# Kernel optimization log

Hardware: AMD Instinct MI355X
Metric: run time of the kernel (lower is better)

The kernel has to match this reference:

```python
import jax, jax.numpy as jnp
import numpy as np

T, B, L, CTX, H = 512, 512, 16, 64, 128
STATE_DIM, SHOT, PID, DATA = 32, 12, 35, 23


def setup_inputs() -> dict:
    key = jax.random.key(0)
    ks = jax.random.split(key, 64)
    k = iter(ks)
    def rn(shape, s=0.1):
        return (jax.random.normal(next(k), shape) * s).astype(jnp.float32)
    xs = jax.random.normal(next(k), (T, B, DATA), jnp.float32)
    xs = xs.at[:, :, 12].set(jax.random.randint(next(k), (T, B), 0, SHOT).astype(jnp.float32))
    xs = xs.at[:, :, 17].set(jax.random.randint(next(k), (T, B), 0, PID).astype(jnp.float32))
    xs = xs.at[:, :, 20].set(jax.random.randint(next(k), (T, B), 0, SHOT).astype(jnp.float32))
    return dict(
        total_xs=jnp.zeros((1,), jnp.float32),
        xs=xs,
        ts=jnp.linspace(0.0, 2.0, T).astype(jnp.float32),
        noise_std=jnp.asarray(0.1, jnp.float32),
        z0_noise=jax.random.normal(next(k), (B, L), jnp.float32),
        bm_noise=jax.random.normal(next(k), (T - 1, B, L), jnp.float32),
        shot_emb=rn((SHOT, 8)), player_emb=rn((PID, 8)),
        gru_wih=rn((3 * H, STATE_DIM)), gru_whh=rn((3 * H, H)),
        gru_bih=rn((3 * H,)), gru_bhh=rn((3 * H,)),
        enc_w=rn((CTX, H)), enc_b=rn((CTX,)),
        qz0_w=rn((2 * L, CTX)), qz0_b=rn((2 * L,)),
        f_w1=rn((H, L + CTX)), f_b1=rn((H,)), f_w2=rn((H, H)), f_b2=rn((H,)),
        f_w3=rn((L, H)), f_b3=rn((L,)),
        h_w1=rn((H, L)), h_b1=rn((H,)), h_w2=rn((H, H)), h_b2=rn((H,)),
        h_w3=rn((L, H)), h_b3=rn((L,)),
        g_w1=rn((L, H)), g_b1=rn((L, H)), g_w2=rn((L, H)), g_b2=rn((L,)),
        proj_w=rn((STATE_DIM, L)), proj_b=rn((STATE_DIM,)),
        pz0_mean=jnp.zeros((1, L), jnp.float32), pz0_logstd=jnp.zeros((1, L), jnp.float32),
        act_w=rn((128, L)), act_b=rn((128,)),
        act_land_w=rn((2, 128)), act_shot_w=rn((SHOT, 128)), act_move_w=rn((2, 128)),
    )


def _forward(xs, noise_std, shot_emb, player_emb, gru_wih, gru_whh, gru_bih, gru_bhh,
             enc_w, enc_b, qz0_w, qz0_b,
             f_w1, f_b1, f_w2, f_b2, f_w3, f_b3,
             h_w1, h_b1, h_w2, h_b2, h_w3, h_b3,
             g_w1, g_b1, g_w2, g_b2,
             proj_w, proj_b, pz0_mean, pz0_logstd,
             act_w, act_b, act_land_w, act_shot_w, act_move_w,
             ts, z0_noise, bm_noise):
    # --- SDE_embed_and_transform: replace shot/player id cols with embeddings ---
    state = xs[:, :, :18]
    shot_ids = state[:, :, 12].astype(jnp.int32)
    pid_ids = state[:, :, 17].astype(jnp.int32)
    state_t = jnp.concatenate([state[:, :, :12], shot_emb[shot_ids],
                               state[:, :, 13:17], player_emb[pid_ids]], axis=-1)  # (T,B,32)
    xs_t = jnp.concatenate([state_t, xs[:, :, 18:]], axis=-1)  # (T,B,37)
    # --- Encoder: GRU over time-reversed states, linear head, flip back ---
    def gru_step(h, xt):
        gi = xt @ gru_wih.T + gru_bih
        gh = h @ gru_whh.T + gru_bhh
        ir, iz, inn = jnp.split(gi, 3, axis=-1)
        hr, hz, hn = jnp.split(gh, 3, axis=-1)
        r = jax.nn.sigmoid(ir + hr)
        zg = jax.nn.sigmoid(iz + hz)
        n = jnp.tanh(inn + r * hn)
        hnew = (1.0 - zg) * n + zg * h
        return hnew, hnew
    h0 = jnp.zeros((xs.shape[1], gru_whh.shape[1]), xs.dtype)
    _, hs = jax.lax.scan(gru_step, h0, state_t[::-1])
    ctx = (hs @ enc_w.T + enc_b)[::-1]  # (T,B,CTX)
    # --- posterior z0 ---
    qm, qls = jnp.split(ctx[0] @ qz0_w.T + qz0_b, 2, axis=1)
    z0 = qm + jnp.exp(qls) * z0_noise
    # --- Euler-Maruyama with logqp; searchsorted(right) -> ctx[min(i+1,T-1)] = ctx[i+1] ---
    dts = ts[1:] - ts[:-1]  # (T-1,)
    dW = jnp.sqrt(dts)[:, None, None] * bm_noise
    ctx_steps = ctx[1:]
    def mlp3(x, w1, b1, w2, b2, w3, b3):
        h1 = jax.nn.softplus(x @ w1.T + b1)
        h2 = jax.nn.softplus(h1 @ w2.T + b2)
        return h2 @ w3.T + b3
    def g_diag(y):  # (B,L): per-latent-dim scalar nets, batched over L
        hg = jax.nn.softplus(y[:, :, None] * g_w1[None] + g_b1[None])  # (B,L,H)
        return jax.nn.sigmoid(jnp.einsum('blh,lh->bl', hg, g_w2) + g_b2)
    def sde_step(z, inp):
        c, dw, dt = inp
        f_val = mlp3(jnp.concatenate([z, c], axis=1), f_w1, f_b1, f_w2, f_b2, f_w3, f_b3)
        h_val = mlp3(z, h_w1, h_b1, h_w2, h_b2, h_w3, h_b3)
        g_val = g_diag(z)
        u = (f_val - h_val) / g_val
        logr = 0.5 * jnp.sum(u * u, axis=1) * dt
        z_new = z + f_val * dt + g_val * dw
        return z_new, (z_new, logr)
    _, (z_tail, log_ratio) = jax.lax.scan(sde_step, z0, (ctx_steps, dW, dts))
    zs = jnp.concatenate([z0[None], z_tail], axis=0)  # (T,B,L)
    _xs = zs @ proj_w.T + proj_b  # (T,B,32)
    # --- action model losses ---
    a = jax.nn.relu(zs @ act_w.T + act_b)
    land = (a @ act_land_w.T).reshape(-1, 2)
    shot_logits = (a @ act_shot_w.T).reshape(-1, act_shot_w.shape[0])
    move = (a @ act_move_w.T).reshape(-1, 2)
    true_actions = xs_t[:, :, -5:]
    true_land = true_actions[:, :, :2].reshape(-1, 2)
    true_move = true_actions[:, :, 3:].reshape(-1, 2)
    true_shot = true_actions[:, :, 2].astype(jnp.int32).reshape(-1)
    land_loss = jnp.mean((land - true_land) ** 2)
    move_loss = jnp.mean((move - true_move) ** 2)
    logp = jax.nn.log_softmax(shot_logits, axis=-1)
    picked = jnp.take_along_axis(logp, true_shot[:, None], axis=1)[:, 0]
    mask = (true_shot != 0).astype(logp.dtype)  # CrossEntropy ignore_index=0
    shot_loss = -jnp.sum(picked * mask) / jnp.maximum(jnp.sum(mask), 1.0)
    # --- reconstruction log-likelihood ---
    xs_state = xs_t[:, :, :STATE_DIM]
    LOG2PI = 1.8378770664093453
    log_pxs = jnp.mean(jnp.sum(
        -0.5 * ((xs_state - _xs) / noise_std) ** 2 - jnp.log(noise_std) - 0.5 * LOG2PI,
        axis=(0, 2)))
    # --- KL(q(z0) || p(z0)) ---
    var_q = jnp.exp(2.0 * qls)
    var_p = jnp.exp(2.0 * pz0_logstd)
    kl = pz0_logstd - qls + (var_q + (qm - pz0_mean) ** 2) / (2.0 * var_p) - 0.5
    logqp0 = jnp.mean(jnp.sum(kl, axis=1))
    logqp_path = jnp.mean(jnp.sum(log_ratio, axis=0))
    return log_pxs, logqp0 + logqp_path + land_loss + shot_loss + move_loss


def reference(total_xs, xs, ts, noise_std, z0_noise, bm_noise, shot_emb, player_emb,
              gru_wih, gru_whh, gru_bih, gru_bhh, enc_w, enc_b, qz0_w, qz0_b,
              f_w1, f_b1, f_w2, f_b2, f_w3, f_b3, h_w1, h_b1, h_w2, h_b2, h_w3, h_b3,
              g_w1, g_b1, g_w2, g_b2, proj_w, proj_b, pz0_mean, pz0_logstd,
              act_w, act_b, act_land_w, act_shot_w, act_move_w):
    return _forward(xs, noise_std, shot_emb, player_emb, gru_wih, gru_whh, gru_bih, gru_bhh,
                    enc_w, enc_b, qz0_w, qz0_b,
                    f_w1, f_b1, f_w2, f_b2, f_w3, f_b3,
                    h_w1, h_b1, h_w2, h_b2, h_w3, h_b3,
                    g_w1, g_b1, g_w2, g_b2,
                    proj_w, proj_b, pz0_mean, pz0_logstd,
                    act_w, act_b, act_land_w, act_shot_w, act_move_w,
                    ts, z0_noise, bm_noise)
```

## Files before the change

kernel.cpp:

```cpp
#include <hip/hip_runtime.h>
#include <cstdint>

typedef _Float16 f16;
typedef _Float16 f16x2 __attribute__((ext_vector_type(2)));

#define T_STEPS 512
#define B_SZ 512
#define LOG2PI 1.8378770664093453f

__device__ __forceinline__ void barrier_lds() {
  asm volatile("s_waitcnt lgkmcnt(0)" ::: "memory");
  __builtin_amdgcn_s_barrier();
  asm volatile("" ::: "memory");
}

__device__ __forceinline__ uint32_t packh2(float a, float b) {
  f16x2 v; v[0] = (f16)a; v[1] = (f16)b;
  return __builtin_bit_cast(uint32_t, v);
}

__device__ __forceinline__ float fdot2(uint32_t a, uint32_t b, float c) {
#if defined(__AMDGCN__) && __has_builtin(__builtin_amdgcn_fdot2)
  return __builtin_amdgcn_fdot2(__builtin_bit_cast(f16x2, a),
                                __builtin_bit_cast(f16x2, b), c, false);
#else
  f16x2 x = __builtin_bit_cast(f16x2, a), y = __builtin_bit_cast(f16x2, b);
  return c + (float)x[0] * (float)y[0] + (float)x[1] * (float)y[1];
#endif
}

#define DOT4(acc, w0, w1, w2, w3, v)                                     \
  do {                                                                   \
    acc = fdot2((w0), (v).x, acc); acc = fdot2((w1), (v).y, acc);        \
    acc = fdot2((w2), (v).z, acc); acc = fdot2((w3), (v).w, acc);        \
  } while (0)

__device__ __forceinline__ float sigmoidf_(float x) {
  return 1.0f / (1.0f + __expf(-x));
}
__device__ __forceinline__ float tanhf_(float x) {
  float ax = fabsf(x);
  float t = __expf(-2.0f * ax);
  float r = (1.0f - t) / (1.0f + t);
  return copysignf(r, x);
}
__device__ __forceinline__ float softplusf_(float x) {
  return fmaxf(x, 0.0f) + __logf(1.0f + __expf(-fabsf(x)));
}

__global__ __launch_bounds__(256) void k_embed(
    const float* __restrict__ xs, const float* __restrict__ shot_emb,
    const float* __restrict__ player_emb, f16* __restrict__ state_t,
    float* __restrict__ accums) {
  if (blockIdx.x == 0 && threadIdx.x < 16) accums[threadIdx.x] = 0.0f;
  size_t idx = (size_t)blockIdx.x * 256 + threadIdx.x;
  const float* xp = xs + idx * 23;
  f16* op = state_t + idx * 32;
  int sid = (int)xp[12];
  int pid = (int)xp[17];
#pragma unroll
  for (int i = 0; i < 12; ++i) op[i] = (f16)xp[i];
  const float* se = shot_emb + sid * 8;
#pragma unroll
  for (int i = 0; i < 8; ++i) op[12 + i] = (f16)se[i];
#pragma unroll
  for (int i = 0; i < 4; ++i) op[20 + i] = (f16)xp[13 + i];
  const float* pe = player_emb + pid * 8;
#pragma unroll
  for (int i = 0; i < 8; ++i) op[24 + i] = (f16)pe[i];
}

__global__ __launch_bounds__(512) void k_gru(
    const f16* __restrict__ state_t, const float* __restrict__ wih,
    const float* __restrict__ whh, const float* __restrict__ bih,
    const float* __restrict__ bhh, const float* __restrict__ enc_w,
    const float* __restrict__ enc_b, const float* __restrict__ qz0_w,
    const float* __restrict__ qz0_b, const float* __restrict__ z0_noise,
    const float* __restrict__ pz0_mean, const float* __restrict__ pz0_logstd,
    f16* __restrict__ ctx, float* __restrict__ z0_out,
    float* __restrict__ accums) {
  __shared__ uint32_t s_x[2][16];
  __shared__ uint32_t s_h[2][64];
  __shared__ float s_gates[2 * 128 * 4];
  __shared__ float s_encp[2 * 64 * 2];
  __shared__ float s_ctx0[2][64];
  __shared__ float s_q[2][32];

  const int tid = threadIdx.x;
  const int bbase = blockIdx.x * 2;
  const uint32_t* stu = (const uint32_t*)state_t;

  uint32_t wA[64];
  uint32_t wB[16];
  float bias0 = 0.f, bias1 = 0.f, encbr = 0.f;

  if (tid < 256) {
    int g = tid >> 7, du = tid & 127;
    const float* whr = whh + (size_t)(g * 128 + du) * 128;
#pragma unroll
    for (int i = 0; i < 64; ++i) wA[i] = packh2(whr[2 * i], whr[2 * i + 1]);
    const float* wxr = wih + (size_t)(g * 128 + du) * 32;
#pragma unroll
    for (int i = 0; i < 16; ++i) wB[i] = packh2(wxr[2 * i], wxr[2 * i + 1]);
    bias0 = bih[g * 128 + du] + bhh[g * 128 + du];
  } else if (tid < 384) {
    int du = tid - 256;
    const float* whr = whh + (size_t)(256 + du) * 128;
#pragma unroll
    for (int i = 0; i < 64; ++i) wA[i] = packh2(whr[2 * i], whr[2 * i + 1]);
    const float* wxr = wih + (size_t)(256 + du) * 32;
#pragma unroll
    for (int i = 0; i < 16; ++i) wB[i] = packh2(wxr[2 * i], wxr[2 * i + 1]);
    bias0 = bih[256 + du];
    bias1 = bhh[256 + du];
  } else {
    int e = tid - 384, c = e & 63, ks = e >> 6;
    const float* wer = enc_w + (size_t)c * 128 + ks * 64;
#pragma unroll
    for (int i = 0; i < 32; ++i) wA[i] = packh2(wer[2 * i], wer[2 * i + 1]);
    encbr = enc_b[c];
  }

  if (tid < 128) s_h[tid >> 6][tid & 63] = 0u;
  if (tid < 32) {
    int b = tid >> 4, i = tid & 15;
    s_x[b][i] = stu[((size_t)(T_STEPS - 1) * B_SZ + bbase + b) * 16 + i];
  }
  float h_old = 0.0f;
  __syncthreads();

  for (int t = T_STEPS - 1; t >= 0; --t) {
    uint4 xpref = make_uint4(0, 0, 0, 0);
    if (tid < 256) {
      int g = tid >> 7, du = tid & 127;
#pragma unroll
      for (int b = 0; b < 2; ++b) {
        float a = bias0;
        const uint4* xq = (const uint4*)&s_x[b][0];
#pragma unroll
        for (int j = 0; j < 4; ++j) {
          uint4 v = xq[j];
          DOT4(a, wB[4 * j], wB[4 * j + 1], wB[4 * j + 2], wB[4 * j + 3], v);
        }
        const uint4* hq = (const uint4*)&s_h[b][0];
#pragma unroll
        for (int j = 0; j < 16; ++j) {
          uint4 v = hq[j];
          DOT4(a, wA[4 * j], wA[4 * j + 1], wA[4 * j + 2], wA[4 * j + 3], v);
        }
        s_gates[(b * 128 + du) * 4 + g] = a;
      }
    } else if (tid < 384) {
      int du = tid - 256;
#pragma unroll
      for (int b = 0; b < 2; ++b) {
        float aI = bias0, aH = bias1;
        const uint4* xq = (const uint4*)&s_x[b][0];
#pragma unroll
        for (int j = 0; j < 4; ++j) {
          uint4 v = xq[j];
          DOT4(aI, wB[4 * j], wB[4 * j + 1], wB[4 * j + 2], wB[4 * j + 3], v);
        }
        const uint4* hq = (const uint4*)&s_h[b][0];
#pragma unroll
        for (int j = 0; j < 16; ++j) {
          uint4 v = hq[j];
          DOT4(aH, wA[4 * j], wA[4 * j + 1], wA[4 * j + 2], wA[4 * j + 3], v);
        }
        s_gates[(b * 128 + du) * 4 + 2] = aI;
        s_gates[(b * 128 + du) * 4 + 3] = aH;
      }
    } else {
      int e = tid - 384, ks = e >> 6, cc = e & 63;
      (void)cc;
      if (t < T_STEPS - 1) {
#pragma unroll
        for (int b = 0; b < 2; ++b) {
          float a = 0.f;
          const uint4* hq = (const uint4*)&s_h[b][ks * 32];
#pragma unroll
          for (int j = 0; j < 8; ++j) {
            uint4 v = hq[j];
            DOT4(a, wA[4 * j], wA[4 * j + 1], wA[4 * j + 2], wA[4 * j + 3], v);
          }
          s_encp[(b * 64 + cc) * 2 + ks] = a;
        }
      }
      if (e < 8 && t > 0) {
        int b = e & 1, q = e >> 1;
        xpref = *(const uint4*)(stu +
                                ((size_t)(t - 1) * B_SZ + bbase + b) * 16 + q * 4);
      }
    }
    barrier_lds();
    if (tid < 256) {
      int b = tid >> 7, du = tid & 127;
      const float4 gt = *(const float4*)&s_gates[(b * 128 + du) * 4];
      float r = sigmoidf_(gt.x), zg = sigmoidf_(gt.y);
      float n = tanhf_(gt.z + r * gt.w);
      float hnew = (1.0f - zg) * n + zg * h_old;
      h_old = hnew;
      ((f16*)&s_h[b][0])[du] = (f16)hnew;
    } else if (tid >= 384) {
      int e = tid - 384, cc = e & 63, b = e >> 6;
      if (t < T_STEPS - 1) {
        float2 p = *(const float2*)&s_encp[(b * 64 + cc) * 2];
        ctx[((size_t)(t + 1) * B_SZ + bbase + b) * 64 + cc] =
            (f16)(p.x + p.y + encbr);
      }
      if (e < 8 && t > 0) {
        int b2 = e & 1, q = e >> 1;
        *(uint4*)&s_x[b2][q * 4] = xpref;
      }
    }
    barrier_lds();
  }

  if (tid >= 384) {
    int e = tid - 384, ks = e >> 6, cc = e & 63;
#pragma unroll
    for (int b = 0; b < 2; ++b) {
      float a = 0.f;
      const uint4* hq = (const uint4*)&s_h[b][ks * 32];
#pragma unroll
      for (int j = 0; j < 8; ++j) {
        uint4 v = hq[j];
        DOT4(a, wA[4 * j], wA[4 * j + 1], wA[4 * j + 2], wA[4 * j + 3], v);
      }
      s_encp[(b * 64 + cc) * 2 + ks] = a;
    }
  }
  __syncthreads();
  if (tid >= 384) {
    int e = tid - 384, cc = e & 63, b = e >> 6;
    float2 p = *(const float2*)&s_encp[(b * 64 + cc) * 2];
    float val = p.x + p.y + encbr;
    ctx[((size_t)bbase + b) * 64 + cc] = (f16)val;
    s_ctx0[b][cc] = val;
  }
  __syncthreads();
  if (tid < 64) {
    int b = tid >> 5, o = tid & 31;
    float acc = qz0_b[o];
#pragma unroll 8
    for (int k = 0; k < 64; ++k) acc += qz0_w[o * 64 + k] * s_ctx0[b][k];
    s_q[b][o] = acc;
  }
  __syncthreads();
  if (tid < 32) {
    int b = tid >> 4, l = tid & 15;
    int bg = bbase + b;
    float qm = s_q[b][l], qls = s_q[b][16 + l];
    float z0v = qm + __expf(qls) * z0_noise[bg * 16 + l];
    z0_out[bg * 16 + l] = z0v;
    float pm = pz0_mean[l], pls = pz0_logstd[l];
    float var_q = __expf(2.0f * qls);
    float var_p = __expf(2.0f * pls);
    float dm = qm - pm;
    float kl = pls - qls + (var_q + dm * dm) / (2.0f * var_p) - 0.5f;
    atomicAdd(&accums[5], kl);
  }
}

__global__ __launch_bounds__(256, 2) void k_sde(
    const f16* __restrict__ ctx, const float* __restrict__ z0_in,
    const float* __restrict__ ts, const float* __restrict__ bm_noise,
    const float* __restrict__ fw1, const float* __restrict__ fb1,
    const float* __restrict__ fw2, const float* __restrict__ fb2,
    const float* __restrict__ fw3, const float* __restrict__ fb3,
    const float* __restrict__ hw1, const float* __restrict__ hb1,
    const float* __restrict__ hw2, const float* __restrict__ hb2,
    const float* __restrict__ hw3, const float* __restrict__ hb3,
    const float* __restrict__ gw1, const float* __restrict__ gb1,
    const float* __restrict__ gw2, const float* __restrict__ gb2,
    f16* __restrict__ zs, float* __restrict__ accums) {
  __shared__ uint32_t s_x2[40];
  __shared__ float s_zf[16];
  __shared__ uint32_t s_h1[2][64];
  __shared__ uint32_t s_h2[2][64];
  __shared__ float s_gp[256];
  __shared__ float s_dts[T_STEPS];

  const int tid = threadIdx.x;
  const int bg = blockIdx.x;
  const uint32_t* cu = (const uint32_t*)ctx;

  uint32_t gw1r[8], gb1r[8], gw2r[8];
  uint32_t uw1[40];
  uint32_t wP2[64];
  uint32_t wP3[32];
  float bias1r = 0.f, bias2r = 0.f, gb2r = 0.f, fb3r = 0.f, hb3r = 0.f;

  {
    int l = tid & 15, kc = tid >> 4;
#pragma unroll
    for (int i = 0; i < 8; ++i) {
      int h = kc * 8 + i;
      gw1r[i] = __builtin_bit_cast(uint32_t, gw1[l * 128 + h]);
      gb1r[i] = __builtin_bit_cast(uint32_t, gb1[l * 128 + h]);
      gw2r[i] = __builtin_bit_cast(uint32_t, gw2[l * 128 + h]);
    }
  }
  if (tid < 128) {
    const float* w = fw1 + (size_t)tid * 80;
#pragma unroll
    for (int i = 0; i < 40; ++i) uw1[i] = packh2(w[2 * i], w[2 * i + 1]);
    bias1r = fb1[tid];
  } else {
    int u = tid - 128;
    const float* w = hw1 + (size_t)u * 16;
#pragma unroll
    for (int i = 0; i < 8; ++i) uw1[i] = packh2(w[2 * i], w[2 * i + 1]);
    bias1r = hb1[u];
  }
  {
    int mlp = tid >> 7, u = tid & 127;
    const float* w = (mlp ? hw2 : fw2) + (size_t)u * 128;
#pragma unroll
    for (int i = 0; i < 64; ++i) wP2[i] = packh2(w[2 * i], w[2 * i + 1]);
    bias2r = (mlp ? hb2 : fb2)[u];
  }
  if (tid < 64) {
    int l = tid >> 2, mlp = (tid >> 1) & 1, kh = tid & 1;
    const float* w = (mlp ? hw3 : fw3) + (size_t)l * 128 + kh * 64;
#pragma unroll
    for (int i = 0; i < 32; ++i) wP3[i] = packh2(w[2 * i], w[2 * i + 1]);
    if ((tid & 3) == 0) {
      gb2r = gb2[l];
      fb3r = fb3[l];
      hb3r = hb3[l];
    }
  }

  for (int i = tid; i < T_STEPS - 1; i += 256) s_dts[i] = ts[i + 1] - ts[i];
  float bmc = 0.f;
  float path_acc = 0.0f;
  uint4 cpref = make_uint4(0, 0, 0, 0);
  if (tid < 64 && (tid & 3) == 0) {
    int l = tid >> 2;
    float z = z0_in[bg * 16 + l];
    s_zf[l] = z;
    ((f16*)&s_x2[0])[l] = (f16)z;
    zs[(size_t)bg * 16 + l] = (f16)z;
    bmc = bm_noise[(size_t)bg * 16 + l];
  }
  if (tid >= 128 && tid < 136) {
    int q = tid - 128;
    uint4 v = *(const uint4*)(cu + ((size_t)1 * B_SZ + bg) * 32 + q * 4);
    *(uint4*)&s_x2[8 + q * 4] = v;
  }
  __syncthreads();

  for (int t = 0; t < T_STEPS - 1; ++t) {
    float bmn = 0.f;
    if (tid < 64 && (tid & 3) == 0 && t < T_STEPS - 2)
      bmn = bm_noise[((size_t)(t + 1) * B_SZ + bg) * 16 + (tid >> 2)];
    if (tid >= 128 && tid < 136 && t <= T_STEPS - 3) {
      int q = tid - 128;
      cpref = *(const uint4*)(cu + ((size_t)(t + 2) * B_SZ + bg) * 32 + q * 4);
    }
    {
      int l = tid & 15;
      float y = s_zf[l];
      float acc = 0.f;
#pragma unroll
      for (int i = 0; i < 8; ++i) {
        float pre = fmaf(y, __builtin_bit_cast(float, gw1r[i]),
                         __builtin_bit_cast(float, gb1r[i]));
        acc = fmaf(softplusf_(pre), __builtin_bit_cast(float, gw2r[i]), acc);
      }
      s_gp[l * 16 + (tid >> 4)] = acc;
    }
    if (tid < 128) {
      float a0 = bias1r, a1 = 0.f;
      const uint4* xq = (const uint4*)&s_x2[0];
#pragma unroll
      for (int j = 0; j < 10; j += 2) {
        uint4 v0 = xq[j], v1 = xq[j + 1];
        DOT4(a0, uw1[4 * j], uw1[4 * j + 1], uw1[4 * j + 2], uw1[4 * j + 3], v0);
        DOT4(a1, uw1[4 * j + 4], uw1[4 * j + 5], uw1[4 * j + 6], uw1[4 * j + 7], v1);
      }
      ((f16*)&s_h1[0][0])[tid] = (f16)softplusf_(a0 + a1);
    } else {
      float a = bias1r;
      const uint4* xq = (const uint4*)&s_x2[0];
#pragma unroll
      for (int j = 0; j < 2; ++j) {
        uint4 v = xq[j];
        DOT4(a, uw1[4 * j], uw1[4 * j + 1], uw1[4 * j + 2], uw1[4 * j + 3], v);
      }
      ((f16*)&s_h1[1][0])[tid - 128] = (f16)softplusf_(a);
    }
    barrier_lds();
    {
      int mlp = tid >> 7, u = tid & 127;
      float a0 = 0.f, a1 = 0.f;
      const uint4* hq = (const uint4*)&s_h1[mlp][0];
#pragma unroll
      for (int j = 0; j < 16; j += 2) {
        uint4 v0 = hq[j], v1 = hq[j + 1];
        DOT4(a0, wP2[4 * j], wP2[4 * j + 1], wP2[4 * j + 2], wP2[4 * j + 3], v0);
        DOT4(a1, wP2[4 * j + 4], wP2[4 * j + 5], wP2[4 * j + 6], wP2[4 * j + 7], v1);
      }
      ((f16*)&s_h2[mlp][0])[u] = (f16)softplusf_(a0 + a1 + bias2r);
    }
    barrier_lds();
    if (tid < 64) {
      int l = tid >> 2, kh = tid & 1;
      int mlp = (tid >> 1) & 1;
      const uint4* hq = (const uint4*)&s_h2[mlp][kh * 32];
      float a0 = 0.f, a1 = 0.f;
#pragma unroll
      for (int j = 0; j < 8; j += 2) {
        uint4 v0 = hq[j], v1 = hq[j + 1];
        DOT4(a0, wP3[4 * j], wP3[4 * j + 1], wP3[4 * j + 2], wP3[4 * j + 3], v0);
        DOT4(a1, wP3[4 * j + 4], wP3[4 * j + 5], wP3[4 * j + 6], wP3[4 * j + 7], v1);
      }
      float a = a0 + a1;
      float full = a + __shfl_xor(a, 1);
      float other = __shfl_xor(full, 2);
      if ((tid & 3) == 0) {
        float fv = full + fb3r;
        float hv = other + hb3r;
        const float4* gp = (const float4*)&s_gp[l * 16];
        float4 g0 = gp[0], g1 = gp[1], g2 = gp[2], g3 = gp[3];
        float gs = g0.x + g0.y + g0.z + g0.w + g1.x + g1.y + g1.z + g1.w +
                   g2.x + g2.y + g2.z + g2.w + g3.x + g3.y + g3.z + g3.w + gb2r;
        float gv = sigmoidf_(gs);
        float dt = s_dts[t];
        float u_ = (fv - hv) / gv;
        float lsum = u_ * u_;
        lsum += __shfl_xor(lsum, 4);
        lsum += __shfl_xor(lsum, 8);
        lsum += __shfl_xor(lsum, 16);
        lsum += __shfl_xor(lsum, 32);
        if (tid == 0) path_acc += 0.5f * lsum * dt;
        float dw = sqrtf(dt) * bmc;
        float zn = s_zf[l] + fv * dt + gv * dw;
        s_zf[l] = zn;
        ((f16*)&s_x2[0])[l] = (f16)zn;
        zs[((size_t)(t + 1) * B_SZ + bg) * 16 + l] = (f16)zn;
        bmc = bmn;
      }
    } else if (tid >= 128 && tid < 136 && t <= T_STEPS - 3) {
      int q = tid - 128;
      *(uint4*)&s_x2[8 + q * 4] = cpref;
    }
    barrier_lds();
  }
  if (tid == 0) atomicAdd(&accums[6], path_acc);
}

__global__ __launch_bounds__(256) void k_dec(
    const f16* __restrict__ zs, const f16* __restrict__ state_t,
    const float* __restrict__ xs, const float* __restrict__ proj_w,
    const float* __restrict__ proj_b, const float* __restrict__ act_w,
    const float* __restrict__ act_b, const float* __restrict__ land_w,
    const float* __restrict__ shot_w, const float* __restrict__ move_w,
    float* __restrict__ accums) {
  __shared__ uint32_t s_proj[8 * 32];
  __shared__ uint32_t s_act[8 * 128];
  __shared__ uint32_t s_head[128 * 8];
  __shared__ float s_pb[32], s_ab[128];
  __shared__ float s_red[4 * 5];

  const int tid = threadIdx.x;
  for (int id = tid; id < 8 * 32; id += 256) {
    int kp = id & 7, n = id >> 3;
    s_proj[kp * 32 + n] = packh2(proj_w[n * 16 + 2 * kp], proj_w[n * 16 + 2 * kp + 1]);
  }
  for (int id = tid; id < 8 * 128; id += 256) {
    int kp = id & 7, n = id >> 3;
    s_act[kp * 128 + n] = packh2(act_w[n * 16 + 2 * kp], act_w[n * 16 + 2 * kp + 1]);
  }
  for (int id = tid; id < 128 * 8; id += 256) {
    int j = id >> 3, p = id & 7;
    int h0 = 2 * p, h1 = 2 * p + 1;
    float w0 = (h0 < 2) ? land_w[h0 * 128 + j]
                        : (h0 < 14 ? shot_w[(h0 - 2) * 128 + j]
                                   : move_w[(h0 - 14) * 128 + j]);
    float w1 = (h1 < 2) ? land_w[h1 * 128 + j]
                        : (h1 < 14 ? shot_w[(h1 - 2) * 128 + j]
                                   : move_w[(h1 - 14) * 128 + j]);
    s_head[j * 8 + p] = packh2(w0, w1);
  }
  if (tid < 32) s_pb[tid] = proj_b[tid];
  if (tid < 128) s_ab[tid] = act_b[tid];
  __syncthreads();

  size_t idx = (size_t)blockIdx.x * 256 + tid;
  uint32_t z2[8];
  const uint32_t* zp = (const uint32_t*)(zs + idx * 16);
#pragma unroll
  for (int i = 0; i < 8; ++i) z2[i] = zp[i];
  uint32_t stv[16];
  const uint32_t* stp = (const uint32_t*)(state_t + idx * 32);
#pragma unroll
  for (int i = 0; i < 16; ++i) stv[i] = stp[i];

  float sqsum = 0.0f;
#pragma unroll 4
  for (int i = 0; i < 32; ++i) {
    float acc = s_pb[i];
#pragma unroll
    for (int kp = 0; kp < 8; ++kp) acc = fdot2(s_proj[kp * 32 + i], z2[kp], acc);
    f16x2 sv = __builtin_bit_cast(f16x2, stv[i >> 1]);
    float d = (float)sv[i & 1] - acc;
    sqsum += d * d;
  }

  float hd[16];
#pragma unroll
  for (int i = 0; i < 16; ++i) hd[i] = 0.0f;
#pragma unroll 2
  for (int j = 0; j < 128; ++j) {
    float a = s_ab[j];
#pragma unroll
    for (int kp = 0; kp < 8; ++kp) a = fdot2(s_act[kp * 128 + j], z2[kp], a);
    a = fmaxf(a, 0.0f);
#pragma unroll
    for (int p = 0; p < 8; ++p) {
      f16x2 w = __builtin_bit_cast(f16x2, s_head[j * 8 + p]);
      hd[2 * p] += (float)w[0] * a;
      hd[2 * p + 1] += (float)w[1] * a;
    }
  }
  const float* xp = xs + idx * 23;
  float dl0 = hd[0] - xp[18], dl1 = hd[1] - xp[19];
  float land = dl0 * dl0 + dl1 * dl1;
  float dm0 = hd[14] - xp[21], dm1 = hd[15] - xp[22];
  float move = dm0 * dm0 + dm1 * dm1;
  int sid = (int)xp[20];
  float m = hd[2];
#pragma unroll
  for (int s = 1; s < 12; ++s) m = fmaxf(m, hd[2 + s]);
  float sume = 0.0f;
#pragma unroll
  for (int s = 0; s < 12; ++s) sume += __expf(hd[2 + s] - m);
  float lse = m + __logf(sume);
  float pl = 0.0f;
#pragma unroll
  for (int s = 0; s < 12; ++s)
    if (s == sid) pl = hd[2 + s];
  float picked = 0.0f, cnt = 0.0f;
  if (sid != 0) {
    picked = pl - lse;
    cnt = 1.0f;
  }
  float vals[5] = {sqsum, land, move, picked, cnt};
#pragma unroll
  for (int v = 0; v < 5; ++v) {
    float x = vals[v];
    for (int off = 1; off < 64; off <<= 1) x += __shfl_xor(x, off);
    vals[v] = x;
  }
  int lane = tid & 63, wv = tid >> 6;
  if (lane == 0) {
#pragma unroll
    for (int v = 0; v < 5; ++v) s_red[wv * 5 + v] = vals[v];
  }
  __syncthreads();
  if (tid == 0) {
#pragma unroll
    for (int v = 0; v < 5; ++v) {
      float s = s_red[v] + s_red[5 + v] + s_red[10 + v] + s_red[15 + v];
      atomicAdd(&accums[v], s);
    }
  }
}

__global__ void k_fin(const float* __restrict__ accums,
                      const float* __restrict__ noise_std,
                      float* __restrict__ out) {
  if (threadIdx.x == 0 && blockIdx.x == 0) {
    float sd = noise_std[0];
    float log_pxs = -0.5f * accums[0] / (sd * sd * (float)B_SZ) -
                    (float)T_STEPS * 32.0f * (logf(sd) + 0.5f * LOG2PI);
    float land = accums[1] / (float)(T_STEPS * B_SZ * 2);
    float move = accums[2] / (float)(T_STEPS * B_SZ * 2);
    float shot = -accums[3] / fmaxf(accums[4], 1.0f);
    float out1 = accums[5] / (float)B_SZ + accums[6] / (float)B_SZ + land + shot + move;
    out[0] = log_pxs;
    out[1] = out1;
  }
}

extern "C" void kernel_launch(void* const* d_in, const int* in_sizes, int n_in,
                              void* d_out, int out_size, void* d_ws,
                              size_t ws_size, hipStream_t stream) {
  const float* xs = (const float*)d_in[1];
  const float* ts = (const float*)d_in[2];
  const float* noise_std = (const float*)d_in[3];
  const float* z0_noise = (const float*)d_in[4];
  const float* bm_noise = (const float*)d_in[5];
  const float* shot_emb = (const float*)d_in[6];
  const float* player_emb = (const float*)d_in[7];
  const float* gru_wih = (const float*)d_in[8];
  const float* gru_whh = (const float*)d_in[9];
  const float* gru_bih = (const float*)d_in[10];
  const float* gru_bhh = (const float*)d_in[11];
  const float* enc_w = (const float*)d_in[12];
  const float* enc_b = (const float*)d_in[13];
  const float* qz0_w = (const float*)d_in[14];
  const float* qz0_b = (const float*)d_in[15];
  const float* f_w1 = (const float*)d_in[16];
  const float* f_b1 = (const float*)d_in[17];
  const float* f_w2 = (const float*)d_in[18];
  const float* f_b2 = (const float*)d_in[19];
  const float* f_w3 = (const float*)d_in[20];
  const float* f_b3 = (const float*)d_in[21];
  const float* h_w1 = (const float*)d_in[22];
  const float* h_b1 = (const float*)d_in[23];
  const float* h_w2 = (const float*)d_in[24];
  const float* h_b2 = (const float*)d_in[25];
  const float* h_w3 = (const float*)d_in[26];
  const float* h_b3 = (const float*)d_in[27];
  const float* g_w1 = (const float*)d_in[28];
  const float* g_b1 = (const float*)d_in[29];
  const float* g_w2 = (const float*)d_in[30];
  const float* g_b2 = (const float*)d_in[31];
  const float* proj_w = (const float*)d_in[32];
  const float* proj_b = (const float*)d_in[33];
  const float* pz0_mean = (const float*)d_in[34];
  const float* pz0_logstd = (const float*)d_in[35];
  const float* act_w = (const float*)d_in[36];
  const float* act_b = (const float*)d_in[37];
  const float* act_land_w = (const float*)d_in[38];
  const float* act_shot_w = (const float*)d_in[39];
  const float* act_move_w = (const float*)d_in[40];

  char* ws = (char*)d_ws;
  float* accums = (float*)ws;
  f16* state_t = (f16*)(ws + 256);
  f16* ctx = (f16*)(ws + 256 + 16777216);
  float* z0b = (float*)(ws + 256 + 16777216 + 33554432);
  f16* zs = (f16*)(ws + 256 + 16777216 + 33554432 + 32768);

  k_embed<<<1024, 256, 0, stream>>>(xs, shot_emb, player_emb, state_t, accums);
  k_gru<<<256, 512, 0, stream>>>(state_t, gru_wih, gru_whh, gru_bih, gru_bhh,
                                 enc_w, enc_b, qz0_w, qz0_b, z0_noise, pz0_mean,
                                 pz0_logstd, ctx, z0b, accums);
  k_sde<<<512, 256, 0, stream>>>(ctx, z0b, ts, bm_noise, f_w1, f_b1, f_w2, f_b2,
                                 f_w3, f_b3, h_w1, h_b1, h_w2, h_b2, h_w3, h_b3,
                                 g_w1, g_b1, g_w2, g_b2, zs, accums);
  k_dec<<<1024, 256, 0, stream>>>(zs, state_t, xs, proj_w, proj_b, act_w, act_b,
                                  act_land_w, act_shot_w, act_move_w, accums);
  k_fin<<<1, 64, 0, stream>>>(accums, noise_std, (float*)d_out);
}
```

Before: 1.934 ms.

## Run SDE solver per batch element in a single wavefront without barriers

Rewrites the SDE integration kernel to use one 64-lane wavefront per batch element instead of 256 threads. Each lane computes two hidden units, so every per-timestep block barrier can be dropped and only compiler memory fences remain. Layer-1, layer-3 and diffusion-net weights move from registers to LDS, while the layer-2 weights (256 packed registers per lane) stay in registers. This removes barrier latency on the serial 511-step critical path, at the cost of more work per lane and high register pressure that could spill.

After: 3.219 ms. 1.66x slower.

```diff
diff --git a/kernel.cpp b/kernel.cpp
--- a/kernel.cpp
+++ b/kernel.cpp
@@ -46,6 +46,9 @@
 }
 __device__ __forceinline__ float softplusf_(float x) {
   return fmaxf(x, 0.0f) + __logf(1.0f + __expf(-fabsf(x)));
+}
+__device__ __forceinline__ float asf_(uint32_t u) {
+  return __builtin_bit_cast(float, u);
 }
 
 __global__ __launch_bounds__(256) void k_embed(
@@ -262,7 +265,7 @@
   }
 }
 
-__global__ __launch_bounds__(256, 2) void k_sde(
+__global__ __launch_bounds__(64, 1) void k_sde(
     const f16* __restrict__ ctx, const float* __restrict__ z0_in,
     const float* __restrict__ ts, const float* __restrict__ bm_noise,
     const float* __restrict__ fw1, const float* __restrict__ fb1,
@@ -274,181 +277,223 @@
     const float* __restrict__ gw1, const float* __restrict__ gb1,
     const float* __restrict__ gw2, const float* __restrict__ gb2,
     f16* __restrict__ zs, float* __restrict__ accums) {
-  __shared__ uint32_t s_x2[40];
+  __shared__ uint4 f1w[64][21];
+  __shared__ uint4 h1w[64][5];
+  __shared__ uint4 f3w[64][5];
+  __shared__ uint4 h3w[64][5];
+  __shared__ uint4 gB[64][25];
+  __shared__ uint4 x2s[10];
+  __shared__ uint4 h1f[16], h1h[16], h2f[16], h2h[16];
   __shared__ float s_zf[16];
-  __shared__ uint32_t s_h1[2][64];
-  __shared__ uint32_t s_h2[2][64];
-  __shared__ float s_gp[256];
   __shared__ float s_dts[T_STEPS];
 
-  const int tid = threadIdx.x;
+  const int ln = threadIdx.x;
   const int bg = blockIdx.x;
-  const uint32_t* cu = (const uint32_t*)ctx;
-
-  uint32_t gw1r[8], gb1r[8], gw2r[8];
-  uint32_t uw1[40];
-  uint32_t wP2[64];
-  uint32_t wP3[32];
-  float bias1r = 0.f, bias2r = 0.f, gb2r = 0.f, fb3r = 0.f, hb3r = 0.f;
+  const int l = ln >> 2, kc = ln & 3;
+  const int r0 = 2 * ln, r1 = 2 * ln + 1;
 
   {
-    int l = tid & 15, kc = tid >> 4;
+    uint32_t* p = (uint32_t*)&f1w[ln][0];
+    const float* wa = fw1 + (size_t)r0 * 80;
+    const float* wb = fw1 + (size_t)r1 * 80;
+#pragma unroll
+    for (int i = 0; i < 40; ++i) {
+      p[i] = packh2(wa[2 * i], wa[2 * i + 1]);
+      p[40 + i] = packh2(wb[2 * i], wb[2 * i + 1]);
+    }
+  }
+  {
+    uint32_t* p = (uint32_t*)&h1w[ln][0];
+    const float* wa = hw1 + (size_t)r0 * 16;
+    const float* wb = hw1 + (size_t)r1 * 16;
 #pragma unroll
     for (int i = 0; i < 8; ++i) {
-      int h = kc * 8 + i;
-      gw1r[i] = __builtin_bit_cast(uint32_t, gw1[l * 128 + h]);
-      gb1r[i] = __builtin_bit_cast(uint32_t, gb1[l * 128 + h]);
-      gw2r[i] = __builtin_bit_cast(uint32_t, gw2[l * 128 + h]);
-    }
-  }
-  if (tid < 128) {
-    const float* w = fw1 + (size_t)tid * 80;
-#pragma unroll
-    for (int i = 0; i < 40; ++i) uw1[i] = packh2(w[2 * i], w[2 * i + 1]);
-    bias1r = fb1[tid];
-  } else {
-    int u = tid - 128;
-    const float* w = hw1 + (size_t)u * 16;
-#pragma unroll
-    for (int i = 0; i < 8; ++i) uw1[i] = packh2(w[2 * i], w[2 * i + 1]);
-    bias1r = hb1[u];
+      p[i] = packh2(wa[2 * i], wa[2 * i + 1]);
+      p[8 + i] = packh2(wb[2 * i], wb[2 * i + 1]);
+    }
   }
   {
-    int mlp = tid >> 7, u = tid & 127;
-    const float* w = (mlp ? hw2 : fw2) + (size_t)u * 128;
-#pragma unroll
-    for (int i = 0; i < 64; ++i) wP2[i] = packh2(w[2 * i], w[2 * i + 1]);
-    bias2r = (mlp ? hb2 : fb2)[u];
-  }
-  if (tid < 64) {
-    int l = tid >> 2, mlp = (tid >> 1) & 1, kh = tid & 1;
-    const float* w = (mlp ? hw3 : fw3) + (size_t)l * 128 + kh * 64;
-#pragma unroll
-    for (int i = 0; i < 32; ++i) wP3[i] = packh2(w[2 * i], w[2 * i + 1]);
-    if ((tid & 3) == 0) {
-      gb2r = gb2[l];
-      fb3r = fb3[l];
-      hb3r = hb3[l];
-    }
-  }
-
-  for (int i = tid; i < T_STEPS - 1; i += 256) s_dts[i] = ts[i + 1] - ts[i];
-  float bmc = 0.f;
-  float path_acc = 0.0f;
+    uint32_t* p = (uint32_t*)&f3w[ln][0];
+    uint32_t* q = (uint32_t*)&h3w[ln][0];
+    const float* wa = fw3 + (size_t)l * 128 + kc * 32;
+    const float* wb = hw3 + (size_t)l * 128 + kc * 32;
+#pragma unroll
+    for (int i = 0; i < 16; ++i) {
+      p[i] = packh2(wa[2 * i], wa[2 * i + 1]);
+      q[i] = packh2(wb[2 * i], wb[2 * i + 1]);
+    }
+  }
+  {
+    float* gp = (float*)&gB[ln][0];
+    const int hb = kc * 32;
+#pragma unroll
+    for (int j = 0; j < 32; ++j) {
+      gp[j] = gw1[l * 128 + hb + j];
+      gp[32 + j] = gb1[l * 128 + hb + j];
+      gp[64 + j] = gw2[l * 128 + hb + j];
+    }
+  }
+  uint4 f2a[16], f2b[16], h2a[16], h2b[16];
+  {
+    const float* wa = fw2 + (size_t)r0 * 128;
+    const float* wb = fw2 + (size_t)r1 * 128;
+    const float* wc = hw2 + (size_t)r0 * 128;
+    const float* wd = hw2 + (size_t)r1 * 128;
+#pragma unroll
+    for (int j = 0; j < 16; ++j) {
+      uint4 u;
+      u.x = packh2(wa[8 * j + 0], wa[8 * j + 1]);
+      u.y = packh2(wa[8 * j + 2], wa[8 * j + 3]);
+      u.z = packh2(wa[8 * j + 4], wa[8 * j + 5]);
+      u.w = packh2(wa[8 * j + 6], wa[8 * j + 7]);
+      f2a[j] = u;
+      u.x = packh2(wb[8 * j + 0], wb[8 * j + 1]);
+      u.y = packh2(wb[8 * j + 2], wb[8 * j + 3]);
+      u.z = packh2(wb[8 * j + 4], wb[8 * j + 5]);
+      u.w = packh2(wb[8 * j + 6], wb[8 * j + 7]);
+      f2b[j] = u;
+      u.x = packh2(wc[8 * j + 0], wc[8 * j + 1]);
+      u.y = packh2(wc[8 * j + 2], wc[8 * j + 3]);
+      u.z = packh2(wc[8 * j + 4], wc[8 * j + 5]);
+      u.w = packh2(wc[8 * j + 6], wc[8 * j + 7]);
+      h2a[j] = u;
+      u.x = packh2(wd[8 * j + 0], wd[8 * j + 1]);
+      u.y = packh2(wd[8 * j + 2], wd[8 * j + 3]);
+      u.z = packh2(wd[8 * j + 4], wd[8 * j + 5]);
+      u.w = packh2(wd[8 * j + 6], wd[8 * j + 7]);
+      h2b[j] = u;
+    }
+  }
+  const float bf1a = fb1[r0], bf1b = fb1[r1];
+  const float bh1a = hb1[r0], bh1b = hb1[r1];
+  const float bf2a = fb2[r0], bf2b = fb2[r1];
+  const float bh2a = hb2[r0], bh2b = hb2[r1];
+  const float fb3r = fb3[l], hb3r = hb3[l], gb2r = gb2[l];
+
+  for (int i = ln; i < T_STEPS - 1; i += 64) s_dts[i] = ts[i + 1] - ts[i];
+
+  const uint4* ctx4 = (const uint4*)ctx;
   uint4 cpref = make_uint4(0, 0, 0, 0);
-  if (tid < 64 && (tid & 3) == 0) {
-    int l = tid >> 2;
+  float bmc = 0.f, bmn = 0.f, path_acc = 0.f;
+  if (kc == 0) {
     float z = z0_in[bg * 16 + l];
     s_zf[l] = z;
-    ((f16*)&s_x2[0])[l] = (f16)z;
+    ((f16*)&x2s[0])[l] = (f16)z;
     zs[(size_t)bg * 16 + l] = (f16)z;
     bmc = bm_noise[(size_t)bg * 16 + l];
   }
-  if (tid >= 128 && tid < 136) {
-    int q = tid - 128;
-    uint4 v = *(const uint4*)(cu + ((size_t)1 * B_SZ + bg) * 32 + q * 4);
-    *(uint4*)&s_x2[8 + q * 4] = v;
-  }
+  if (ln < 8) cpref = ctx4[((size_t)1 * B_SZ + bg) * 8 + ln];
   __syncthreads();
 
   for (int t = 0; t < T_STEPS - 1; ++t) {
-    float bmn = 0.f;
-    if (tid < 64 && (tid & 3) == 0 && t < T_STEPS - 2)
-      bmn = bm_noise[((size_t)(t + 1) * B_SZ + bg) * 16 + (tid >> 2)];
-    if (tid >= 128 && tid < 136 && t <= T_STEPS - 3) {
-      int q = tid - 128;
-      cpref = *(const uint4*)(cu + ((size_t)(t + 2) * B_SZ + bg) * 32 + q * 4);
-    }
+    if (ln < 8) x2s[2 + ln] = cpref;
+    if (kc == 0 && t < T_STEPS - 2)
+      bmn = bm_noise[((size_t)(t + 1) * B_SZ + bg) * 16 + l];
+    if (ln < 8 && t <= T_STEPS - 3)
+      cpref = ctx4[((size_t)(t + 2) * B_SZ + bg) * 8 + ln];
+    asm volatile("" ::: "memory");
+
+    float y = s_zf[l];
+    float gacc = 0.f;
+#pragma unroll
+    for (int q = 0; q < 8; ++q) {
+      uint4 w1q = gB[ln][q], b1q = gB[ln][8 + q], w2q = gB[ln][16 + q];
+      gacc = fmaf(softplusf_(fmaf(y, asf_(w1q.x), asf_(b1q.x))), asf_(w2q.x), gacc);
+      gacc = fmaf(softplusf_(fmaf(y, asf_(w1q.y), asf_(b1q.y))), asf_(w2q.y), gacc);
+      gacc = fmaf(softplusf_(fmaf(y, asf_(w1q.z), asf_(b1q.z))), asf_(w2q.z), gacc);
+      gacc = fmaf(softplusf_(fmaf(y, asf_(w1q.w), asf_(b1q.w))), asf_(w2q.w), gacc);
+    }
+    gacc += __shfl_xor(gacc, 1);
+    gacc += __shfl_xor(gacc, 2);
+
+    float a00 = bf1a, a01 = 0.f, a10 = bf1b, a11 = 0.f;
+#pragma unroll
+    for (int j = 0; j < 10; ++j) {
+      uint4 xv = x2s[j];
+      uint4 w0 = f1w[ln][j];
+      uint4 w1v = f1w[ln][10 + j];
+      if (j & 1) {
+        DOT4(a01, w0.x, w0.y, w0.z, w0.w, xv);
+        DOT4(a11, w1v.x, w1v.y, w1v.z, w1v.w, xv);
+      } else {
+        DOT4(a00, w0.x, w0.y, w0.z, w0.w, xv);
+        DOT4(a10, w1v.x, w1v.y, w1v.z, w1v.w, xv);
+      }
+    }
+    ((uint32_t*)h1f)[ln] = packh2(softplusf_(a00 + a01), softplusf_(a10 + a11));
+    float c0 = bh1a, c1 = bh1b;
     {
-      int l = tid & 15;
-      float y = s_zf[l];
-      float acc = 0.f;
-#pragma unroll
-      for (int i = 0; i < 8; ++i) {
-        float pre = fmaf(y, __builtin_bit_cast(float, gw1r[i]),
-                         __builtin_bit_cast(float, gb1r[i]));
-        acc = fmaf(softplusf_(pre), __builtin_bit_cast(float, gw2r[i]), acc);
-      }
-      s_gp[l * 16 + (tid >> 4)] = acc;
-    }
-    if (tid < 128) {
-      float a0 = bias1r, a1 = 0.f;
-      const uint4* xq = (const uint4*)&s_x2[0];
-#pragma unroll
-      for (int j = 0; j < 10; j += 2) {
-        uint4 v0 = xq[j], v1 = xq[j + 1];
-        DOT4(a0, uw1[4 * j], uw1[4 * j + 1], uw1[4 * j + 2], uw1[4 * j + 3], v0);
-        DOT4(a1, uw1[4 * j + 4], uw1[4 * j + 5], uw1[4 * j + 6], uw1[4 * j + 7], v1);
-      }
-      ((f16*)&s_h1[0][0])[tid] = (f16)softplusf_(a0 + a1);
-    } else {
-      float a = bias1r;
-      const uint4* xq = (const uint4*)&s_x2[0];
-#pragma unroll
-      for (int j = 0; j < 2; ++j) {
-        uint4 v = xq[j];
-        DOT4(a, uw1[4 * j], uw1[4 * j + 1], uw1[4 * j + 2], uw1[4 * j + 3], v);
-      }
-      ((f16*)&s_h1[1][0])[tid - 128] = (f16)softplusf_(a);
-    }
-    barrier_lds();
-    {
-      int mlp = tid >> 7, u = tid & 127;
-      float a0 = 0.f, a1 = 0.f;
-      const uint4* hq = (const uint4*)&s_h1[mlp][0];
-#pragma unroll
-      for (int j = 0; j < 16; j += 2) {
-        uint4 v0 = hq[j], v1 = hq[j + 1];
-        DOT4(a0, wP2[4 * j], wP2[4 * j + 1], wP2[4 * j + 2], wP2[4 * j + 3], v0);
-        DOT4(a1, wP2[4 * j + 4], wP2[4 * j + 5], wP2[4 * j + 6], wP2[4 * j + 7], v1);
-      }
-      ((f16*)&s_h2[mlp][0])[u] = (f16)softplusf_(a0 + a1 + bias2r);
-    }
-    barrier_lds();
-    if (tid < 64) {
-      int l = tid >> 2, kh = tid & 1;
-      int mlp = (tid >> 1) & 1;
-      const uint4* hq = (const uint4*)&s_h2[mlp][kh * 32];
-      float a0 = 0.f, a1 = 0.f;
-#pragma unroll
-      for (int j = 0; j < 8; j += 2) {
-        uint4 v0 = hq[j], v1 = hq[j + 1];
-        DOT4(a0, wP3[4 * j], wP3[4 * j + 1], wP3[4 * j + 2], wP3[4 * j + 3], v0);
-        DOT4(a1, wP3[4 * j + 4], wP3[4 * j + 5], wP3[4 * j + 6], wP3[4 * j + 7], v1);
-      }
-      float a = a0 + a1;
-      float full = a + __shfl_xor(a, 1);
-      float other = __shfl_xor(full, 2);
-      if ((tid & 3) == 0) {
-        float fv = full + fb3r;
-        float hv = other + hb3r;
-        const float4* gp = (const float4*)&s_gp[l * 16];
-        float4 g0 = gp[0], g1 = gp[1], g2 = gp[2], g3 = gp[3];
-        float gs = g0.x + g0.y + g0.z + g0.w + g1.x + g1.y + g1.z + g1.w +
-                   g2.x + g2.y + g2.z + g2.w + g3.x + g3.y + g3.z + g3.w + gb2r;
-        float gv = sigmoidf_(gs);
-        float dt = s_dts[t];
-        float u_ = (fv - hv) / gv;
-        float lsum = u_ * u_;
-        lsum += __shfl_xor(lsum, 4);
-        lsum += __shfl_xor(lsum, 8);
-        lsum += __shfl_xor(lsum, 16);
-        lsum += __shfl_xor(lsum, 32);
-        if (tid == 0) path_acc += 0.5f * lsum * dt;
-        float dw = sqrtf(dt) * bmc;
-        float zn = s_zf[l] + fv * dt + gv * dw;
-        s_zf[l] = zn;
-        ((f16*)&s_x2[0])[l] = (f16)zn;
-        zs[((size_t)(t + 1) * B_SZ + bg) * 16 + l] = (f16)zn;
-        bmc = bmn;
-      }
-    } else if (tid >= 128 && tid < 136 && t <= T_STEPS - 3) {
-      int q = tid - 128;
-      *(uint4*)&s_x2[8 + q * 4] = cpref;
-    }
-    barrier_lds();
-  }
-  if (tid == 0) atomicAdd(&accums[6], path_acc);
+      uint4 xv = x2s[0];
+      uint4 wz0 = h1w[ln][0], wz2 = h1w[ln][2];
+      DOT4(c0, wz0.x, wz0.y, wz0.z, wz0.w, xv);
+      DOT4(c1, wz2.x, wz2.y, wz2.z, wz2.w, xv);
+      xv = x2s[1];
+      uint4 wz1 = h1w[ln][1], wz3 = h1w[ln][3];
+      DOT4(c0, wz1.x, wz1.y, wz1.z, wz1.w, xv);
+      DOT4(c1, wz3.x, wz3.y, wz3.z, wz3.w, xv);
+    }
+    ((uint32_t*)h1h)[ln] = packh2(softplusf_(c0), softplusf_(c1));
+    asm volatile("" ::: "memory");
+
+    float d00 = bf2a, d01 = 0.f, d10 = bf2b, d11 = 0.f;
+    float e00 = bh2a, e01 = 0.f, e10 = bh2b, e11 = 0.f;
+#pragma unroll
+    for (int j = 0; j < 16; ++j) {
+      uint4 vf = h1f[j];
+      uint4 vh = h1h[j];
+      if (j & 1) {
+        DOT4(d01, f2a[j].x, f2a[j].y, f2a[j].z, f2a[j].w, vf);
+        DOT4(d11, f2b[j].x, f2b[j].y, f2b[j].z, f2b[j].w, vf);
+        DOT4(e01, h2a[j].x, h2a[j].y, h2a[j].z, h2a[j].w, vh);
+        DOT4(e11, h2b[j].x, h2b[j].y, h2b[j].z, h2b[j].w, vh);
+      } else {
+        DOT4(d00, f2a[j].x, f2a[j].y, f2a[j].z, f2a[j].w, vf);
+        DOT4(d10, f2b[j].x, f2b[j].y, f2b[j].z, f2b[j].w, vf);
+        DOT4(e00, h2a[j].x, h2a[j].y, h2a[j].z, h2a[j].w, vh);
+        DOT4(e10, h2b[j].x, h2b[j].y, h2b[j].z, h2b[j].w, vh);
+      }
+    }
+    ((uint32_t*)h2f)[ln] = packh2(softplusf_(d00 + d01), softplusf_(d10 + d11));
+    ((uint32_t*)h2h)[ln] = packh2(softplusf_(e00 + e01), softplusf_(e10 + e11));
+    asm volatile("" ::: "memory");
+
+    float p3 = 0.f, q3 = 0.f;
+#pragma unroll
+    for (int j = 0; j < 4; ++j) {
+      uint4 vf = h2f[kc * 4 + j];
+      uint4 wf = f3w[ln][j];
+      DOT4(p3, wf.x, wf.y, wf.z, wf.w, vf);
+      uint4 vh = h2h[kc * 4 + j];
+      uint4 wh = h3w[ln][j];
+      DOT4(q3, wh.x, wh.y, wh.z, wh.w, vh);
+    }
+    p3 += __shfl_xor(p3, 1);
+    p3 += __shfl_xor(p3, 2);
+    q3 += __shfl_xor(q3, 1);
+    q3 += __shfl_xor(q3, 2);
+
+    if (kc == 0) {
+      float fv = p3 + fb3r;
+      float hv = q3 + hb3r;
+      float gv = sigmoidf_(gacc + gb2r);
+      float dt = s_dts[t];
+      float u_ = (fv - hv) / gv;
+      float lsum = u_ * u_;
+      lsum += __shfl_xor(lsum, 4);
+      lsum += __shfl_xor(lsum, 8);
+      lsum += __shfl_xor(lsum, 16);
+      lsum += __shfl_xor(lsum, 32);
+      if (ln == 0) path_acc += 0.5f * lsum * dt;
+      float dw = sqrtf(dt) * bmc;
+      float zn = s_zf[l] + fv * dt + gv * dw;
+      s_zf[l] = zn;
+      ((f16*)&x2s[0])[l] = (f16)zn;
+      zs[((size_t)(t + 1) * B_SZ + bg) * 16 + l] = (f16)zn;
+      bmc = bmn;
+    }
+    asm volatile("" ::: "memory");
+  }
+  if (ln == 0) atomicAdd(&accums[6], path_acc);
 }
 
 __global__ __launch_bounds__(256) void k_dec(
@@ -640,9 +685,9 @@
   k_gru<<<256, 512, 0, stream>>>(state_t, gru_wih, gru_whh, gru_bih, gru_bhh,
                                  enc_w, enc_b, qz0_w, qz0_b, z0_noise, pz0_mean,
                                  pz0_logstd, ctx, z0b, accums);
-  k_sde<<<512, 256, 0, stream>>>(ctx, z0b, ts, bm_noise, f_w1, f_b1, f_w2, f_b2,
-                                 f_w3, f_b3, h_w1, h_b1, h_w2, h_b2, h_w3, h_b3,
-                                 g_w1, g_b1, g_w2, g_b2, zs, accums);
+  k_sde<<<512, 64, 0, stream>>>(ctx, z0b, ts, bm_noise, f_w1, f_b1, f_w2, f_b2,
+                                f_w3, f_b3, h_w1, h_b1, h_w2, h_b2, h_w3, h_b3,
+                                g_w1, g_b1, g_w2, g_b2, zs, accums);
   k_dec<<<1024, 256, 0, stream>>>(zs, state_t, xs, proj_w, proj_b, act_w, act_b,
                                   act_land_w, act_shot_w, act_move_w, accums);
   k_fin<<<1, 64, 0, stream>>>(accums, noise_std, (float*)d_out);
```
